# Optimization experiments

Measured on AMD Instinct MI355X. Metric: run time of the kernel, lower is better.

## Reference

```python
import jax, jax.numpy as jnp
import numpy as np

N0, N1, N2, N3 = 262144, 65536, 16384, 4096
EPS = 1e-5  # BatchNorm1d default eps


def setup_inputs() -> dict:
    key = jax.random.key(0)
    ks = jax.random.split(key, 10)
    f0 = jax.random.normal(ks[0], (N0, 64), dtype=jnp.float32)
    f1 = jax.random.normal(ks[1], (N1, 128), dtype=jnp.float32)
    f2 = jax.random.normal(ks[2], (N2, 256), dtype=jnp.float32)
    f3 = jax.random.normal(ks[3], (N3, 512), dtype=jnp.float32)
    # upsampling indices: finer level gathers from coarser level
    idx0 = jax.random.randint(ks[4], (N2,), 0, N3, dtype=jnp.int32)   # f3 -> level2
    idx1 = jax.random.randint(ks[5], (N1,), 0, N2, dtype=jnp.int32)   # f2 -> level1
    idx2 = jax.random.randint(ks[6], (N0,), 0, N1, dtype=jnp.int32)   # f1 -> level0
    # BN weight init'd to constant 0.25 in the module; bias defaults to 0
    bn_w2, bn_b2 = jnp.full((512,), 0.25, jnp.float32), jnp.zeros((512,), jnp.float32)
    bn_w1, bn_b1 = jnp.full((256,), 0.25, jnp.float32), jnp.zeros((256,), jnp.float32)
    bn_w0, bn_b0 = jnp.full((128,), 0.25, jnp.float32), jnp.zeros((128,), jnp.float32)
    # Linear(in, out, bias=False) weights, torch layout [out, in]
    W2 = jax.random.normal(ks[7], (256, 512), dtype=jnp.float32) * 0.02
    W1 = jax.random.normal(ks[8], (128, 256), dtype=jnp.float32) * 0.02
    W0 = jax.random.normal(ks[9], (64, 128), dtype=jnp.float32) * 0.02
    return dict(f0=f0, f1=f1, f2=f2, f3=f3,
                bn_w2=bn_w2, bn_b2=bn_b2, W2=W2,
                bn_w1=bn_w1, bn_b1=bn_b1, W1=W1,
                bn_w0=bn_w0, bn_b0=bn_b0, W0=W0,
                idx0=idx0, idx1=idx1, idx2=idx2)


def _decode(f, bn_w, bn_b, W):
    # BatchNorm1d (training-mode batch stats, biased variance) -> Linear (no bias)
    mean = jnp.mean(f, axis=0)
    var = jnp.var(f, axis=0)
    xn = (f - mean) * jax.lax.rsqrt(var + EPS)
    return (xn * bn_w + bn_b) @ W.T  # [N, out_ch]


def reference(f0, f1, f2, f3, bn_w2, bn_b2, W2, bn_w1, bn_b1, W1,
              bn_w0, bn_b0, W0, idx0, idx1, idx2):
    # gather (upsample) -> BN -> Linear -> residual add, coarse to fine
    f2 = f2 + _decode(f3[idx0], bn_w2, bn_b2, W2)   # [N2, 256]
    f1 = f1 + _decode(f2[idx1], bn_w1, bn_b1, W1)   # [N1, 128]
    f0 = f0 + _decode(f1[idx2], bn_w0, bn_b0, W0)   # [N0, 64]
    return f0
```

## Files before the change

### kernel.cpp

```cpp
#include <hip/hip_runtime.h>
#include <hip/hip_cooperative_groups.h>

namespace cg = cooperative_groups;

#define BN_EPS 1e-5f

constexpr int PN0 = 262144, PN1 = 65536, PN2 = 16384, PN3 = 4096;
constexpr int NBLK = 256, NTHR = 256;
constexpr size_t MB = 1u << 20;

typedef __attribute__((ext_vector_type(8))) short short8;
typedef __attribute__((ext_vector_type(4))) float f32x4;
typedef __attribute__((ext_vector_type(4))) unsigned int u32x4;

typedef const __attribute__((address_space(1))) unsigned int gu32;
typedef __attribute__((address_space(3))) unsigned int lu32;

__device__ __forceinline__ unsigned f2bf(float f) {
    unsigned u = __builtin_bit_cast(unsigned, f);
    u += 0x7fff + ((u >> 16) & 1);
    return u >> 16;
}
__device__ __forceinline__ float bf2f(unsigned h) {
    return __builtin_bit_cast(float, h << 16);
}
__device__ __forceinline__ f32x4 ntload4(const float* p) {
    return __builtin_nontemporal_load(reinterpret_cast<const f32x4*>(p));
}
__device__ __forceinline__ void ntstore4(float* p, f32x4 v) {
    __builtin_nontemporal_store(v, reinterpret_cast<f32x4*>(p));
}

struct MegaArgs {
    const float *f0, *f1, *f2, *f3;
    const float *bnw2, *bnb2, *W2;
    const float *bnw1, *bnb1, *W1;
    const float *bnw0, *bnb0, *W0;
    const int *idx0, *idx1, *idx2;
    unsigned short *f3bf, *dec2, *dec1, *dec0, *f2p, *f1p, *Wp2, *Wp1, *Wp0;
    int *cnt3, *cnt2, *cnt1;
    float *part2, *part1, *part0;
    float *d2, *d1, *d0;
    float *out;
};

template<int G, int NL>
__device__ __forceinline__ void red_write(float* aux, const float s[8], const float q[8],
                                          int tid, int lr, int cgi,
                                          float* part, int vb, int C) {
    #pragma unroll
    for (int j = 0; j < 8; ++j) aux[(lr * G + cgi) * 8 + j] = s[j];
    __syncthreads();
    if (tid < G) {
        float ss[8] = {};
        for (int l = 0; l < NL; ++l)
            #pragma unroll
            for (int j = 0; j < 8; ++j) ss[j] += aux[(l * G + tid) * 8 + j];
        #pragma unroll
        for (int j = 0; j < 8; ++j)
            part[((size_t)vb * C + tid * 8 + j) * 2] = ss[j];
    }
    __syncthreads();
    #pragma unroll
    for (int j = 0; j < 8; ++j) aux[(lr * G + cgi) * 8 + j] = q[j];
    __syncthreads();
    if (tid < G) {
        float qq[8] = {};
        for (int l = 0; l < NL; ++l)
            #pragma unroll
            for (int j = 0; j < 8; ++j) qq[j] += aux[(l * G + tid) * 8 + j];
        #pragma unroll
        for (int j = 0; j < 8; ++j)
            part[((size_t)vb * C + tid * 8 + j) * 2 + 1] = qq[j];
    }
    __syncthreads();
}

__device__ void phase_hist(const MegaArgs& a, int bid, int tid) {
    if (bid < 64) {
        atomicAdd(&a.cnt3[a.idx0[bid * NTHR + tid]], 1);
    } else {
        int t = (bid - 64) * NTHR + tid;
        atomicAdd(&a.cnt2[a.idx1[t]], 1);
        int t2 = t + 49152;
        if (t2 < PN1) atomicAdd(&a.cnt2[a.idx1[t2]], 1);
    }
}

__device__ void phase_stats(const MegaArgs& a, int bid, int tid, float* aux) {
    if (bid < 128) {
        const int cgi = tid & 63, lr = tid >> 6;
        const int r0 = bid * 32;
        float s[8] = {}, q[8] = {};
        #pragma unroll
        for (int i = 0; i < 8; ++i) {
            int r = r0 + lr + 4 * i;
            float w = (float)a.cnt3[r];
            const float* p = a.f3 + (size_t)r * 512 + cgi * 8;
            float4 x0 = *reinterpret_cast<const float4*>(p);
            float4 x1 = *reinterpret_cast<const float4*>(p + 4);
            float v[8] = {x0.x, x0.y, x0.z, x0.w, x1.x, x1.y, x1.z, x1.w};
            uint4 o;
            o.x = f2bf(v[0]) | (f2bf(v[1]) << 16);
            o.y = f2bf(v[2]) | (f2bf(v[3]) << 16);
            o.z = f2bf(v[4]) | (f2bf(v[5]) << 16);
            o.w = f2bf(v[6]) | (f2bf(v[7]) << 16);
            *reinterpret_cast<uint4*>(a.f3bf + (size_t)r * 512 + cgi * 8) = o;
            #pragma unroll
            for (int j = 0; j < 8; ++j) { s[j] += w * v[j]; q[j] += w * v[j] * v[j]; }
        }
        red_write<64, 4>(aux, s, q, tid, lr, cgi, a.part2, bid, 512);
    } else {
        int base = (bid - 128) * 2048;
        #pragma unroll
        for (int i = 0; i < 8; ++i)
            atomicAdd(&a.cnt1[a.idx2[base + i * NTHR + tid]], 1);
    }
}

template<int K, int NB>
__device__ void prep_phase(int bid, int tid, const float* part,
                           const float* bnw, const float* bnb, float invN,
                           const float* W, unsigned short* Wp, float* d,
                           float* aux) {
    float* sc = aux;
    float* sh = aux + K;
    for (int c = tid; c < K; c += NTHR) {
        float s = 0.f, q = 0.f;
        for (int b = 0; b < NB; ++b) {
            float2 p = *reinterpret_cast<const float2*>(part + ((size_t)b * K + c) * 2);
            s += p.x;
            q += p.y;
        }
        float mean = s * invN;
        float var = fmaxf(q * invN - mean * mean, 0.f);
        float scl = bnw[c] * rsqrtf(var + BN_EPS);
        sc[c] = scl;
        sh[c] = bnb[c] - mean * scl;
    }
    __syncthreads();
    const int nl = tid >> 4;
    const int kc = tid & 15;
    const int n = bid * 16 + nl;
    const int cb = n >> 6, n64 = n & 63;
    const float* wrow = W + (size_t)n * K;
    unsigned short* wp = Wp + (size_t)cb * 64 * K;
    float dp = 0.f;
    #pragma unroll
    for (int i = 0; i < K / 128; ++i) {
        int k = kc * 8 + i * 128;
        float4 w0 = *reinterpret_cast<const float4*>(wrow + k);
        float4 w1 = *reinterpret_cast<const float4*>(wrow + k + 4);
        float4 s0 = *reinterpret_cast<const float4*>(&sc[k]);
        float4 s1 = *reinterpret_cast<const float4*>(&sc[k + 4]);
        float4 h0 = *reinterpret_cast<const float4*>(&sh[k]);
        float4 h1 = *reinterpret_cast<const float4*>(&sh[k + 4]);
        dp += h0.x * w0.x + h0.y * w0.y + h0.z * w0.z + h0.w * w0.w
            + h1.x * w1.x + h1.y * w1.y + h1.z * w1.z + h1.w * w1.w;
        uint4 o;
        o.x = f2bf(w0.x * s0.x) | (f2bf(w0.y * s0.y) << 16);
        o.y = f2bf(w0.z * s0.z) | (f2bf(w0.w * s0.w) << 16);
        o.z = f2bf(w1.x * s1.x) | (f2bf(w1.y * s1.y) << 16);
        o.w = f2bf(w1.z * s1.z) | (f2bf(w1.w * s1.w) << 16);
        int si = (n64 * K + k) ^ ((n64 & 7) << 3);
        *reinterpret_cast<uint4*>(wp + si) = o;
    }
    dp += __shfl_xor(dp, 1); dp += __shfl_xor(dp, 2);
    dp += __shfl_xor(dp, 4); dp += __shfl_xor(dp, 8);
    if (kc == 0) d[n] = dp;
}

template<int K, int C>
__device__ void gemm_one(int chunk, int panel, int tid,
                         const unsigned short* src, const unsigned short* Wp,
                         const float* dvec, unsigned short* dec,
                         unsigned short* Wl) {
    constexpr int KK = K / 32;
    constexpr int CH = K / 8;
    const int lane = tid & 63;
    const int wv = tid >> 6;
    const int l15 = lane & 15, lg = lane >> 4;
    const int ncol0 = panel * 64;

    {
        const char* g = (const char*)(Wp + (size_t)panel * 64 * K);
        char* l = (char*)Wl;
        #pragma unroll
        for (int i = 0; i < CH / 4; ++i) {
            int ch = i * 4 + wv;
            __builtin_amdgcn_global_load_lds((gu32*)(g + ch * 1024 + lane * 16),
                                             (lu32*)(l + ch * 1024 + lane * 16), 16, 0, 0);
        }
    }

    const int row = chunk * 64 + wv * 16 + l15;
    const unsigned short* xp = src + (size_t)row * K + lg * 8;
    short8 xf[KK];
    #pragma unroll
    for (int kk = 0; kk < KK; ++kk)
        xf[kk] = *reinterpret_cast<const short8*>(xp + kk * 32);

    float4 dr[4];
    #pragma unroll
    for (int ni = 0; ni < 4; ++ni)
        dr[ni] = *reinterpret_cast<const float4*>(&dvec[ncol0 + ni * 16 + lg * 4]);

    __syncthreads();

    f32x4 acc[4];
    #pragma unroll
    for (int ni = 0; ni < 4; ++ni) acc[ni] = (f32x4){0.f, 0.f, 0.f, 0.f};
    #pragma unroll
    for (int kk = 0; kk < KK; ++kk) {
        #pragma unroll
        for (int ni = 0; ni < 4; ++ni) {
            const int si = ((ni * 16 + l15) * K + kk * 32 + lg * 8) ^ ((l15 & 7) << 3);
            short8 wf = *reinterpret_cast<const short8*>(&Wl[si]);
            acc[ni] = __builtin_amdgcn_mfma_f32_16x16x32_bf16(wf, xf[kk], acc[ni], 0, 0, 0);
        }
    }

    const size_t rowoff = (size_t)row * C + ncol0;
    #pragma unroll
    for (int ni = 0; ni < 4; ++ni) {
        size_t off = rowoff + ni * 16 + lg * 4;
        float v0 = dr[ni].x + acc[ni][0];
        float v1 = dr[ni].y + acc[ni][1];
        float v2 = dr[ni].z + acc[ni][2];
        float v3 = dr[ni].w + acc[ni][3];
        *reinterpret_cast<uint2*>(&dec[off]) =
            make_uint2(f2bf(v0) | (f2bf(v1) << 16), f2bf(v2) | (f2bf(v3) << 16));
    }
}

__device__ void phase_gemm1(const MegaArgs& a, int bid, int tid, unsigned short* Wl) {
    constexpr int K = 256;
    const int lane = tid & 63;
    const int wv = tid >> 6;
    const int l15 = lane & 15, lg = lane >> 4;

    {
        const char* g = (const char*)a.Wp1;
        char* l = (char*)Wl;
        #pragma unroll
        for (int i = 0; i < 16; ++i) {
            int ch = i * 4 + wv;
            __builtin_amdgcn_global_load_lds((gu32*)(g + ch * 1024 + lane * 16),
                                             (lu32*)(l + ch * 1024 + lane * 16), 16, 0, 0);
        }
    }

    const int row = bid * 64 + wv * 16 + l15;
    const unsigned short* xp = a.f2p + (size_t)row * K + lg * 8;
    short8 xf[8];
    #pragma unroll
    for (int kk = 0; kk < 8; ++kk)
        xf[kk] = *reinterpret_cast<const short8*>(xp + kk * 32);

    __syncthreads();

    #pragma unroll
    for (int p = 0; p < 2; ++p) {
        const unsigned short* wb = Wl + p * 64 * K;
        f32x4 acc[4];
        #pragma unroll
        for (int ni = 0; ni < 4; ++ni) acc[ni] = (f32x4){0.f, 0.f, 0.f, 0.f};
        #pragma unroll
        for (int kk = 0; kk < 8; ++kk) {
            #pragma unroll
            for (int ni = 0; ni < 4; ++ni) {
                const int si = ((ni * 16 + l15) * K + kk * 32 + lg * 8) ^ ((l15 & 7) << 3);
                short8 wf = *reinterpret_cast<const short8*>(&wb[si]);
                acc[ni] = __builtin_amdgcn_mfma_f32_16x16x32_bf16(wf, xf[kk], acc[ni], 0, 0, 0);
            }
        }
        const int ncol0 = p * 64;
        const size_t rowoff = (size_t)row * 128 + ncol0;
        #pragma unroll
        for (int ni = 0; ni < 4; ++ni) {
            float4 dr = *reinterpret_cast<const float4*>(&a.d1[ncol0 + ni * 16 + lg * 4]);
            size_t off = rowoff + ni * 16 + lg * 4;
            float v0 = dr.x + acc[ni][0];
            float v1 = dr.y + acc[ni][1];
            float v2 = dr.z + acc[ni][2];
            float v3 = dr.w + acc[ni][3];
            *reinterpret_cast<uint2*>(&a.dec1[off]) =
                make_uint2(f2bf(v0) | (f2bf(v1) << 16), f2bf(v2) | (f2bf(v3) << 16));
        }
    }
}

__device__ void phase_gemm0(const MegaArgs& a, int bid, int tid, unsigned short* Wl) {
    constexpr int K = 128;
    const int lane = tid & 63;
    const int wv = tid >> 6;
    const int l15 = lane & 15, lg = lane >> 4;

    {
        const char* g = (const char*)a.Wp0;
        char* l = (char*)Wl;
        #pragma unroll
        for (int i = 0; i < 4; ++i) {
            int ch = i * 4 + wv;
            __builtin_amdgcn_global_load_lds((gu32*)(g + ch * 1024 + lane * 16),
                                             (lu32*)(l + ch * 1024 + lane * 16), 16, 0, 0);
        }
    }
    float4 dr[4];
    #pragma unroll
    for (int ni = 0; ni < 4; ++ni)
        dr[ni] = *reinterpret_cast<const float4*>(&a.d0[ni * 16 + lg * 4]);
    __syncthreads();

    #pragma unroll
    for (int c = 0; c < 4; ++c) {
        const int row = (bid * 4 + c) * 64 + wv * 16 + l15;
        const unsigned short* xp = a.f1p + (size_t)row * K + lg * 8;
        short8 xf[4];
        #pragma unroll
        for (int kk = 0; kk < 4; ++kk)
            xf[kk] = *reinterpret_cast<const short8*>(xp + kk * 32);
        f32x4 acc[4];
        #pragma unroll
        for (int ni = 0; ni < 4; ++ni) acc[ni] = (f32x4){0.f, 0.f, 0.f, 0.f};
        #pragma unroll
        for (int kk = 0; kk < 4; ++kk) {
            #pragma unroll
            for (int ni = 0; ni < 4; ++ni) {
                const int si = ((ni * 16 + l15) * K + kk * 32 + lg * 8) ^ ((l15 & 7) << 3);
                short8 wf = *reinterpret_cast<const short8*>(&Wl[si]);
                acc[ni] = __builtin_amdgcn_mfma_f32_16x16x32_bf16(wf, xf[kk], acc[ni], 0, 0, 0);
            }
        }
        const size_t rowoff = (size_t)row * 64;
        #pragma unroll
        for (int ni = 0; ni < 4; ++ni) {
            size_t off = rowoff + ni * 16 + lg * 4;
            float v0 = dr[ni].x + acc[ni][0];
            float v1 = dr[ni].y + acc[ni][1];
            float v2 = dr[ni].z + acc[ni][2];
            float v3 = dr[ni].w + acc[ni][3];
            *reinterpret_cast<uint2*>(&a.dec0[off]) =
                make_uint2(f2bf(v0) | (f2bf(v1) << 16), f2bf(v2) | (f2bf(v3) << 16));
        }
    }
}

template<int C, int IT, bool STATS, bool OUT_F32>
__device__ void ga_phase(int vb, int tid, const float* base,
                         const unsigned short* dec, const int* idx,
                         const int* cnt_next, void* outv, float* part,
                         float* aux) {
    constexpr int G = C / 8;
    constexpr int NL = 256 / G;
    const int cgi = tid % G;
    const int lr = tid / G;
    const int r0 = vb * (NL * IT);

    int g[IT];
    #pragma unroll
    for (int i = 0; i < IT; ++i) g[i] = idx[r0 + lr + NL * i];

    float wreg[IT];
    if constexpr (STATS) {
        #pragma unroll
        for (int i = 0; i < IT; ++i) wreg[i] = (float)cnt_next[r0 + lr + NL * i];
    }

    u32x4 dv[IT];
    #pragma unroll
    for (int i = 0; i < IT; ++i)
        dv[i] = *reinterpret_cast<const u32x4*>(dec + (size_t)g[i] * C + cgi * 8);

    f32x4 b0[IT], b1[IT];
    #pragma unroll
    for (int i = 0; i < IT; ++i) {
        const float* bp = base + (size_t)(r0 + lr + NL * i) * C + cgi * 8;
        b0[i] = ntload4(bp);
        b1[i] = ntload4(bp + 4);
    }

    float s[8] = {}, q[8] = {};
    #pragma unroll
    for (int i = 0; i < IT; ++i) {
        const int r = r0 + lr + NL * i;
        float v[8];
        v[0] = b0[i][0] + bf2f(dv[i][0] & 0xffffu);
        v[1] = b0[i][1] + bf2f(dv[i][0] >> 16);
        v[2] = b0[i][2] + bf2f(dv[i][1] & 0xffffu);
        v[3] = b0[i][3] + bf2f(dv[i][1] >> 16);
        v[4] = b1[i][0] + bf2f(dv[i][2] & 0xffffu);
        v[5] = b1[i][1] + bf2f(dv[i][2] >> 16);
        v[6] = b1[i][2] + bf2f(dv[i][3] & 0xffffu);
        v[7] = b1[i][3] + bf2f(dv[i][3] >> 16);
        if constexpr (OUT_F32) {
            float* op = (float*)outv + (size_t)r * C + cgi * 8;
            ntstore4(op, (f32x4){v[0], v[1], v[2], v[3]});
            ntstore4(op + 4, (f32x4){v[4], v[5], v[6], v[7]});
        } else {
            unsigned h[8];
            #pragma unroll
            for (int j = 0; j < 8; ++j) h[j] = f2bf(v[j]);
            u32x4 o = {h[0] | (h[1] << 16), h[2] | (h[3] << 16),
                       h[4] | (h[5] << 16), h[6] | (h[7] << 16)};
            *reinterpret_cast<u32x4*>((unsigned short*)outv + (size_t)r * C + cgi * 8) = o;
            if constexpr (STATS) {
                #pragma unroll
                for (int j = 0; j < 8; ++j) {
                    float rv = bf2f(h[j]);
                    s[j] += wreg[i] * rv;
                    q[j] += wreg[i] * rv * rv;
                }
            }
        }
    }

    if constexpr (STATS)
        red_write<G, NL>(aux, s, q, tid, lr, cgi, part, vb, C);
}

__global__ __launch_bounds__(NTHR, 1) void mega(MegaArgs a) {
    __shared__ unsigned short Wl[64 * 512];
    __shared__ float aux[2048];
    cg::grid_group gg = cg::this_grid();
    const int bid = blockIdx.x;
    const int tid = threadIdx.x;

    phase_hist(a, bid, tid);
    __threadfence(); gg.sync(); __threadfence();

    phase_stats(a, bid, tid, aux);
    __threadfence(); gg.sync(); __threadfence();

    if (bid < 16)
        prep_phase<512, 128>(bid, tid, a.part2, a.bnw2, a.bnb2, 1.f / PN2, a.W2, a.Wp2, a.d2, aux);
    __threadfence(); gg.sync(); __threadfence();

    gemm_one<512, 256>(bid & 63, bid >> 6, tid, a.f3bf, a.Wp2, a.d2, a.dec2, Wl);
    __threadfence(); gg.sync(); __threadfence();

    ga_phase<256, 4, true, false>(bid * 2, tid, a.f2, a.dec2, a.idx0, a.cnt2, a.f2p, a.part1, aux);
    ga_phase<256, 4, true, false>(bid * 2 + 1, tid, a.f2, a.dec2, a.idx0, a.cnt2, a.f2p, a.part1, aux);
    __threadfence(); gg.sync(); __threadfence();

    if (bid < 8)
        prep_phase<256, 512>(bid, tid, a.part1, a.bnw1, a.bnb1, 1.f / PN1, a.W1, a.Wp1, a.d1, aux);
    __threadfence(); gg.sync(); __threadfence();

    phase_gemm1(a, bid, tid, Wl);
    __threadfence(); gg.sync(); __threadfence();

    ga_phase<128, 8, true, false>(bid * 2, tid, a.f1, a.dec1, a.idx1, a.cnt1, a.f1p, a.part0, aux);
    ga_phase<128, 8, true, false>(bid * 2 + 1, tid, a.f1, a.dec1, a.idx1, a.cnt1, a.f1p, a.part0, aux);
    __threadfence(); gg.sync(); __threadfence();

    if (bid < 4)
        prep_phase<128, 512>(bid, tid, a.part0, a.bnw0, a.bnb0, 1.f / PN0, a.W0, a.Wp0, a.d0, aux);
    __threadfence(); gg.sync(); __threadfence();

    phase_gemm0(a, bid, tid, Wl);
    __threadfence(); gg.sync(); __threadfence();

    #pragma unroll
    for (int c = 0; c < 4; ++c)
        ga_phase<64, 8, false, true>(bid * 4 + c, tid, a.f0, a.dec0, a.idx2, nullptr, a.out,
                                     nullptr, aux);
}

__global__ __launch_bounds__(NTHR) void k_hist(MegaArgs a) {
    phase_hist(a, blockIdx.x, threadIdx.x);
}
__global__ __launch_bounds__(NTHR) void k_stats(MegaArgs a) {
    __shared__ float aux[2048];
    phase_stats(a, blockIdx.x, threadIdx.x, aux);
}
template<int K, int NB>
__global__ __launch_bounds__(NTHR) void k_prep(const float* part, const float* bnw,
                                               const float* bnb, float invN, const float* W,
                                               unsigned short* Wp, float* d) {
    __shared__ float aux[2048];
    prep_phase<K, NB>(blockIdx.x, threadIdx.x, part, bnw, bnb, invN, W, Wp, d, aux);
}
__global__ __launch_bounds__(NTHR) void k_gemm2(MegaArgs a) {
    __shared__ unsigned short Wl[64 * 512];
    gemm_one<512, 256>(blockIdx.x & 63, blockIdx.x >> 6, threadIdx.x, a.f3bf, a.Wp2, a.d2,
                       a.dec2, Wl);
}
__global__ __launch_bounds__(NTHR) void k_gemm1(MegaArgs a) {
    __shared__ unsigned short Wl[64 * 512];
    phase_gemm1(a, blockIdx.x, threadIdx.x, Wl);
}
__global__ __launch_bounds__(NTHR) void k_gemm0(MegaArgs a) {
    __shared__ unsigned short Wl[64 * 128];
    phase_gemm0(a, blockIdx.x, threadIdx.x, Wl);
}
__global__ __launch_bounds__(NTHR) void k_ga2(MegaArgs a) {
    __shared__ float aux[2048];
    ga_phase<256, 4, true, false>(blockIdx.x * 2, threadIdx.x, a.f2, a.dec2, a.idx0, a.cnt2,
                                  a.f2p, a.part1, aux);
    ga_phase<256, 4, true, false>(blockIdx.x * 2 + 1, threadIdx.x, a.f2, a.dec2, a.idx0, a.cnt2,
                                  a.f2p, a.part1, aux);
}
__global__ __launch_bounds__(NTHR) void k_ga1(MegaArgs a) {
    __shared__ float aux[2048];
    ga_phase<128, 8, true, false>(blockIdx.x * 2, threadIdx.x, a.f1, a.dec1, a.idx1, a.cnt1,
                                  a.f1p, a.part0, aux);
    ga_phase<128, 8, true, false>(blockIdx.x * 2 + 1, threadIdx.x, a.f1, a.dec1, a.idx1, a.cnt1,
                                  a.f1p, a.part0, aux);
}
__global__ __launch_bounds__(NTHR) void k_ga0(MegaArgs a) {
    #pragma unroll
    for (int c = 0; c < 4; ++c)
        ga_phase<64, 8, false, true>(blockIdx.x * 4 + c, threadIdx.x, a.f0, a.dec0, a.idx2,
                                     nullptr, a.out, nullptr, nullptr);
}

extern "C" void kernel_launch(void* const* d_in, const int* in_sizes, int n_in,
                              void* d_out, int out_size, void* d_ws, size_t ws_size,
                              hipStream_t stream) {
    char* wsb = (char*)d_ws;
    unsigned short* f3bf = (unsigned short*)wsb;
    unsigned short* dec2 = (unsigned short*)(wsb + 4 * MB);
    unsigned short* dec1 = (unsigned short*)(wsb + 6 * MB);
    unsigned short* dec0 = (unsigned short*)(wsb + 10 * MB);
    unsigned short* f2p  = (unsigned short*)(wsb + 18 * MB);
    unsigned short* f1p  = (unsigned short*)(wsb + 26 * MB);
    unsigned short* Wp2  = (unsigned short*)(wsb + 42 * MB);
    unsigned short* Wp1  = Wp2 + 4 * 64 * 512;
    unsigned short* Wp0  = Wp1 + 2 * 64 * 256;
    int* cnt3 = (int*)(Wp0 + 64 * 128);
    int* cnt2 = cnt3 + PN3;
    int* cnt1 = cnt2 + PN2;
    float* part2 = (float*)(cnt1 + PN1);
    float* part1 = part2 + 256 * 512 * 2;
    float* part0 = part1 + 512 * 256 * 2;
    float* d2 = part0 + 1024 * 128 * 2;
    float* d1 = d2 + 256;
    float* d0 = d1 + 128;

    MegaArgs a;
    a.f0 = (const float*)d_in[0];
    a.f1 = (const float*)d_in[1];
    a.f2 = (const float*)d_in[2];
    a.f3 = (const float*)d_in[3];
    a.bnw2 = (const float*)d_in[4];
    a.bnb2 = (const float*)d_in[5];
    a.W2 = (const float*)d_in[6];
    a.bnw1 = (const float*)d_in[7];
    a.bnb1 = (const float*)d_in[8];
    a.W1 = (const float*)d_in[9];
    a.bnw0 = (const float*)d_in[10];
    a.bnb0 = (const float*)d_in[11];
    a.W0 = (const float*)d_in[12];
    a.idx0 = (const int*)d_in[13];
    a.idx1 = (const int*)d_in[14];
    a.idx2 = (const int*)d_in[15];
    a.f3bf = f3bf; a.dec2 = dec2; a.dec1 = dec1; a.dec0 = dec0;
    a.f2p = f2p; a.f1p = f1p; a.Wp2 = Wp2; a.Wp1 = Wp1; a.Wp0 = Wp0;
    a.cnt3 = cnt3; a.cnt2 = cnt2; a.cnt1 = cnt1;
    a.part2 = part2; a.part1 = part1; a.part0 = part0;
    a.d2 = d2; a.d1 = d1; a.d0 = d0;
    a.out = (float*)d_out;

    hipMemsetAsync(cnt3, 0, (size_t)(PN3 + PN2 + PN1) * sizeof(int), stream);

    int dev = 0;
    hipGetDevice(&dev);
    int coop = 0;
    hipDeviceGetAttribute(&coop, hipDeviceAttributeCooperativeLaunch, dev);
    int maxb = 0;
    hipOccupancyMaxActiveBlocksPerMultiprocessor(&maxb, mega, NTHR, 0);

    if (coop && maxb >= 1) {
        void* kargs[] = {&a};
        hipLaunchCooperativeKernel((void*)mega, dim3(NBLK), dim3(NTHR), kargs, 0, stream);
    } else {
        k_hist<<<256, NTHR, 0, stream>>>(a);
        k_stats<<<256, NTHR, 0, stream>>>(a);
        k_prep<512, 128><<<16, NTHR, 0, stream>>>(a.part2, a.bnw2, a.bnb2, 1.f / PN2, a.W2,
                                                  a.Wp2, a.d2);
        k_gemm2<<<256, NTHR, 0, stream>>>(a);
        k_ga2<<<256, NTHR, 0, stream>>>(a);
        k_prep<256, 512><<<8, NTHR, 0, stream>>>(a.part1, a.bnw1, a.bnb1, 1.f / PN1, a.W1,
                                                 a.Wp1, a.d1);
        k_gemm1<<<256, NTHR, 0, stream>>>(a);
        k_ga1<<<256, NTHR, 0, stream>>>(a);
        k_prep<128, 512><<<4, NTHR, 0, stream>>>(a.part0, a.bnw0, a.bnb0, 1.f / PN0, a.W0,
                                                 a.Wp0, a.d0);
        k_gemm0<<<256, NTHR, 0, stream>>>(a);
        k_ga0<<<256, NTHR, 0, stream>>>(a);
    }
}
```

Before: 168.0 us.

## Raise cooperative grid occupancy with grid-stride phases and smaller LDS footprint

```diff
diff --git a/kernel.cpp b/kernel.cpp
--- a/kernel.cpp
+++ b/kernel.cpp
@@ -6,7 +6,7 @@
 #define BN_EPS 1e-5f
 
 constexpr int PN0 = 262144, PN1 = 65536, PN2 = 16384, PN3 = 4096;
-constexpr int NBLK = 256, NTHR = 256;
+constexpr int NTHR = 256;
 constexpr size_t MB = 1u << 20;
 
 typedef __attribute__((ext_vector_type(8))) short short8;
@@ -38,7 +38,7 @@
     const float *bnw0, *bnb0, *W0;
     const int *idx0, *idx1, *idx2;
     unsigned short *f3bf, *dec2, *dec1, *dec0, *f2p, *f1p, *Wp2, *Wp1, *Wp0;
-    int *cnt3, *cnt2, *cnt1;
+    int *cnt2, *cnt1;
     float *part2, *part1, *part0;
     float *d2, *d1, *d0;
     float *out;
@@ -76,45 +76,58 @@
     __syncthreads();
 }
 
-__device__ void phase_hist(const MegaArgs& a, int bid, int tid) {
-    if (bid < 64) {
-        atomicAdd(&a.cnt3[a.idx0[bid * NTHR + tid]], 1);
-    } else {
-        int t = (bid - 64) * NTHR + tid;
-        atomicAdd(&a.cnt2[a.idx1[t]], 1);
-        int t2 = t + 49152;
-        if (t2 < PN1) atomicAdd(&a.cnt2[a.idx1[t2]], 1);
-    }
-}
-
-__device__ void phase_stats(const MegaArgs& a, int bid, int tid, float* aux) {
-    if (bid < 128) {
-        const int cgi = tid & 63, lr = tid >> 6;
-        const int r0 = bid * 32;
-        float s[8] = {}, q[8] = {};
-        #pragma unroll
-        for (int i = 0; i < 8; ++i) {
-            int r = r0 + lr + 4 * i;
-            float w = (float)a.cnt3[r];
-            const float* p = a.f3 + (size_t)r * 512 + cgi * 8;
-            float4 x0 = *reinterpret_cast<const float4*>(p);
-            float4 x1 = *reinterpret_cast<const float4*>(p + 4);
-            float v[8] = {x0.x, x0.y, x0.z, x0.w, x1.x, x1.y, x1.z, x1.w};
-            uint4 o;
-            o.x = f2bf(v[0]) | (f2bf(v[1]) << 16);
-            o.y = f2bf(v[2]) | (f2bf(v[3]) << 16);
-            o.z = f2bf(v[4]) | (f2bf(v[5]) << 16);
-            o.w = f2bf(v[6]) | (f2bf(v[7]) << 16);
-            *reinterpret_cast<uint4*>(a.f3bf + (size_t)r * 512 + cgi * 8) = o;
+__device__ void stats_gathered(const MegaArgs& a, int vb, int tid, float* aux) {
+    const int cgi = tid & 63, lr = tid >> 6;
+    const int r0 = vb * 128;
+    float s[8] = {}, q[8] = {};
+    for (int i = 0; i < 32; ++i) {
+        int r = r0 + lr + 4 * i;
+        int gi = a.idx0[r];
+        const float* p = a.f3 + (size_t)gi * 512 + cgi * 8;
+        float4 x0 = *reinterpret_cast<const float4*>(p);
+        float4 x1 = *reinterpret_cast<const float4*>(p + 4);
+        float v[8] = {x0.x, x0.y, x0.z, x0.w, x1.x, x1.y, x1.z, x1.w};
+        #pragma unroll
+        for (int j = 0; j < 8; ++j) { s[j] += v[j]; q[j] += v[j] * v[j]; }
+    }
+    red_write<64, 4>(aux, s, q, tid, lr, cgi, a.part2, vb, 512);
+}
+
+__device__ void cvt_f3(const MegaArgs& a, int vb, int tid) {
+    const int cgi = tid & 63, lr = tid >> 6;
+    const int r0 = vb * 32;
+    #pragma unroll
+    for (int i = 0; i < 8; ++i) {
+        int r = r0 + lr + 4 * i;
+        const float* p = a.f3 + (size_t)r * 512 + cgi * 8;
+        float4 x0 = *reinterpret_cast<const float4*>(p);
+        float4 x1 = *reinterpret_cast<const float4*>(p + 4);
+        uint4 o;
+        o.x = f2bf(x0.x) | (f2bf(x0.y) << 16);
+        o.y = f2bf(x0.z) | (f2bf(x0.w) << 16);
+        o.z = f2bf(x1.x) | (f2bf(x1.y) << 16);
+        o.w = f2bf(x1.z) | (f2bf(x1.w) << 16);
+        *reinterpret_cast<uint4*>(a.f3bf + (size_t)r * 512 + cgi * 8) = o;
+    }
+}
+
+__device__ void phase1(const MegaArgs& a, int nb, int bid, int tid, float* aux) {
+    for (int vb = bid; vb < 416; vb += nb) {
+        if (vb < 128) {
+            stats_gathered(a, vb, tid, aux);
+        } else if (vb < 256) {
+            cvt_f3(a, vb - 128, tid);
+        } else if (vb < 288) {
+            int b = vb - 256;
             #pragma unroll
-            for (int j = 0; j < 8; ++j) { s[j] += w * v[j]; q[j] += w * v[j] * v[j]; }
-        }
-        red_write<64, 4>(aux, s, q, tid, lr, cgi, a.part2, bid, 512);
-    } else {
-        int base = (bid - 128) * 2048;
-        #pragma unroll
-        for (int i = 0; i < 8; ++i)
-            atomicAdd(&a.cnt1[a.idx2[base + i * NTHR + tid]], 1);
+            for (int i = 0; i < 8; ++i)
+                atomicAdd(&a.cnt2[a.idx1[b * 2048 + i * NTHR + tid]], 1);
+        } else {
+            int b = vb - 288;
+            #pragma unroll
+            for (int i = 0; i < 8; ++i)
+                atomicAdd(&a.cnt1[a.idx2[b * 2048 + i * NTHR + tid]], 1);
+        }
     }
 }
 
@@ -168,6 +181,86 @@
     dp += __shfl_xor(dp, 1); dp += __shfl_xor(dp, 2);
     dp += __shfl_xor(dp, 4); dp += __shfl_xor(dp, 8);
     if (kc == 0) d[n] = dp;
+    __syncthreads();
+}
+
+__device__ void gemm2_one(int chunk, int panel, int tid,
+                          const unsigned short* src, const unsigned short* Wp,
+                          const float* dvec, unsigned short* dec,
+                          unsigned short* Wl) {
+    constexpr int K = 512;
+    const int lane = tid & 63;
+    const int wv = tid >> 6;
+    const int l15 = lane & 15, lg = lane >> 4;
+    const char* gbase = (const char*)(Wp + (size_t)panel * 64 * K);
+    char* lbase = (char*)Wl;
+
+    #pragma unroll
+    for (int i = 0; i < 8; ++i) {
+        int ch = i * 4 + wv;
+        __builtin_amdgcn_global_load_lds((gu32*)(gbase + ch * 1024 + lane * 16),
+                                         (lu32*)(lbase + ch * 1024 + lane * 16), 16, 0, 0);
+    }
+
+    const int row = chunk * 64 + wv * 16 + l15;
+    const unsigned short* xp = src + (size_t)row * K + lg * 8;
+    short8 xf[16];
+    #pragma unroll
+    for (int kk = 0; kk < 16; ++kk)
+        xf[kk] = *reinterpret_cast<const short8*>(xp + kk * 32);
+
+    float4 dr[4];
+    #pragma unroll
+    for (int ni = 0; ni < 4; ++ni)
+        dr[ni] = *reinterpret_cast<const float4*>(&dvec[panel * 64 + ni * 16 + lg * 4]);
+
+    __syncthreads();
+
+    f32x4 acc[4];
+    #pragma unroll
+    for (int ni = 0; ni < 4; ++ni) acc[ni] = (f32x4){0.f, 0.f, 0.f, 0.f};
+
+    #pragma unroll
+    for (int kk = 0; kk < 16; ++kk) {
+        #pragma unroll
+        for (int ni = 0; ni < 2; ++ni) {
+            const int si = ((ni * 16 + l15) * K + kk * 32 + lg * 8) ^ ((l15 & 7) << 3);
+            short8 wf = *reinterpret_cast<const short8*>(&Wl[si]);
+            acc[ni] = __builtin_amdgcn_mfma_f32_16x16x32_bf16(wf, xf[kk], acc[ni], 0, 0, 0);
+        }
+    }
+    __syncthreads();
+
+    #pragma unroll
+    for (int i = 0; i < 8; ++i) {
+        int ch = i * 4 + wv;
+        __builtin_amdgcn_global_load_lds((gu32*)(gbase + 32768 + ch * 1024 + lane * 16),
+                                         (lu32*)(lbase + ch * 1024 + lane * 16), 16, 0, 0);
+    }
+    __syncthreads();
+
+    #pragma unroll
+    for (int kk = 0; kk < 16; ++kk) {
+        #pragma unroll
+        for (int ni = 0; ni < 2; ++ni) {
+            const int si = ((ni * 16 + l15) * K + kk * 32 + lg * 8) ^ ((l15 & 7) << 3);
+            short8 wf = *reinterpret_cast<const short8*>(&Wl[si]);
+            acc[2 + ni] = __builtin_amdgcn_mfma_f32_16x16x32_bf16(wf, xf[kk], acc[2 + ni], 0, 0, 0);
+        }
+    }
+
+    const size_t rowoff = (size_t)row * 256 + panel * 64;
+    #pragma unroll
+    for (int ni = 0; ni < 4; ++ni) {
+        size_t off = rowoff + ni * 16 + lg * 4;
+        float v0 = dr[ni].x + acc[ni][0];
+        float v1 = dr[ni].y + acc[ni][1];
+        float v2 = dr[ni].z + acc[ni][2];
+        float v3 = dr[ni].w + acc[ni][3];
+        *reinterpret_cast<uint2*>(&dec[off]) =
+            make_uint2(f2bf(v0) | (f2bf(v1) << 16), f2bf(v2) | (f2bf(v3) << 16));
+    }
+    __syncthreads();
 }
 
 template<int K, int C>
@@ -231,66 +324,10 @@
         *reinterpret_cast<uint2*>(&dec[off]) =
             make_uint2(f2bf(v0) | (f2bf(v1) << 16), f2bf(v2) | (f2bf(v3) << 16));
     }
-}
-
-__device__ void phase_gemm1(const MegaArgs& a, int bid, int tid, unsigned short* Wl) {
-    constexpr int K = 256;
-    const int lane = tid & 63;
-    const int wv = tid >> 6;
-    const int l15 = lane & 15, lg = lane >> 4;
-
-    {
-        const char* g = (const char*)a.Wp1;
-        char* l = (char*)Wl;
-        #pragma unroll
-        for (int i = 0; i < 16; ++i) {
-            int ch = i * 4 + wv;
-            __builtin_amdgcn_global_load_lds((gu32*)(g + ch * 1024 + lane * 16),
-                                             (lu32*)(l + ch * 1024 + lane * 16), 16, 0, 0);
-        }
-    }
-
-    const int row = bid * 64 + wv * 16 + l15;
-    const unsigned short* xp = a.f2p + (size_t)row * K + lg * 8;
-    short8 xf[8];
-    #pragma unroll
-    for (int kk = 0; kk < 8; ++kk)
-        xf[kk] = *reinterpret_cast<const short8*>(xp + kk * 32);
-
-    __syncthreads();
-
-    #pragma unroll
-    for (int p = 0; p < 2; ++p) {
-        const unsigned short* wb = Wl + p * 64 * K;
-        f32x4 acc[4];
-        #pragma unroll
-        for (int ni = 0; ni < 4; ++ni) acc[ni] = (f32x4){0.f, 0.f, 0.f, 0.f};
-        #pragma unroll
-        for (int kk = 0; kk < 8; ++kk) {
-            #pragma unroll
-            for (int ni = 0; ni < 4; ++ni) {
-                const int si = ((ni * 16 + l15) * K + kk * 32 + lg * 8) ^ ((l15 & 7) << 3);
-                short8 wf = *reinterpret_cast<const short8*>(&wb[si]);
-                acc[ni] = __builtin_amdgcn_mfma_f32_16x16x32_bf16(wf, xf[kk], acc[ni], 0, 0, 0);
-            }
-        }
-        const int ncol0 = p * 64;
-        const size_t rowoff = (size_t)row * 128 + ncol0;
-        #pragma unroll
-        for (int ni = 0; ni < 4; ++ni) {
-            float4 dr = *reinterpret_cast<const float4*>(&a.d1[ncol0 + ni * 16 + lg * 4]);
-            size_t off = rowoff + ni * 16 + lg * 4;
-            float v0 = dr.x + acc[ni][0];
-            float v1 = dr.y + acc[ni][1];
-            float v2 = dr.z + acc[ni][2];
-            float v3 = dr.w + acc[ni][3];
-            *reinterpret_cast<uint2*>(&a.dec1[off]) =
-                make_uint2(f2bf(v0) | (f2bf(v1) << 16), f2bf(v2) | (f2bf(v3) << 16));
-        }
-    }
-}
-
-__device__ void phase_gemm0(const MegaArgs& a, int bid, int tid, unsigned short* Wl) {
+    __syncthreads();
+}
+
+__device__ void phase_gemm0(const MegaArgs& a, int nb, int bid, int tid, unsigned short* Wl) {
     constexpr int K = 128;
     const int lane = tid & 63;
     const int wv = tid >> 6;
@@ -312,9 +349,8 @@
         dr[ni] = *reinterpret_cast<const float4*>(&a.d0[ni * 16 + lg * 4]);
     __syncthreads();
 
-    #pragma unroll
-    for (int c = 0; c < 4; ++c) {
-        const int row = (bid * 4 + c) * 64 + wv * 16 + l15;
+    for (int vb = bid; vb < 1024; vb += nb) {
+        const int row = vb * 64 + wv * 16 + l15;
         const unsigned short* xp = a.f1p + (size_t)row * K + lg * 8;
         short8 xf[4];
         #pragma unroll
@@ -419,60 +455,57 @@
         red_write<G, NL>(aux, s, q, tid, lr, cgi, part, vb, C);
 }
 
-__global__ __launch_bounds__(NTHR, 1) void mega(MegaArgs a) {
-    __shared__ unsigned short Wl[64 * 512];
+#define FENCE_SYNC { __threadfence(); gg.sync(); __threadfence(); }
+
+__global__ __launch_bounds__(NTHR, 3) void mega(MegaArgs a) {
+    __shared__ unsigned short Wl[64 * 256];
     __shared__ float aux[2048];
     cg::grid_group gg = cg::this_grid();
+    const int nb = gridDim.x;
     const int bid = blockIdx.x;
     const int tid = threadIdx.x;
 
-    phase_hist(a, bid, tid);
-    __threadfence(); gg.sync(); __threadfence();
-
-    phase_stats(a, bid, tid, aux);
-    __threadfence(); gg.sync(); __threadfence();
-
-    if (bid < 16)
-        prep_phase<512, 128>(bid, tid, a.part2, a.bnw2, a.bnb2, 1.f / PN2, a.W2, a.Wp2, a.d2, aux);
-    __threadfence(); gg.sync(); __threadfence();
-
-    gemm_one<512, 256>(bid & 63, bid >> 6, tid, a.f3bf, a.Wp2, a.d2, a.dec2, Wl);
-    __threadfence(); gg.sync(); __threadfence();
-
-    ga_phase<256, 4, true, false>(bid * 2, tid, a.f2, a.dec2, a.idx0, a.cnt2, a.f2p, a.part1, aux);
-    ga_phase<256, 4, true, false>(bid * 2 + 1, tid, a.f2, a.dec2, a.idx0, a.cnt2, a.f2p, a.part1, aux);
-    __threadfence(); gg.sync(); __threadfence();
-
-    if (bid < 8)
-        prep_phase<256, 512>(bid, tid, a.part1, a.bnw1, a.bnb1, 1.f / PN1, a.W1, a.Wp1, a.d1, aux);
-    __threadfence(); gg.sync(); __threadfence();
-
-    phase_gemm1(a, bid, tid, Wl);
-    __threadfence(); gg.sync(); __threadfence();
-
-    ga_phase<128, 8, true, false>(bid * 2, tid, a.f1, a.dec1, a.idx1, a.cnt1, a.f1p, a.part0, aux);
-    ga_phase<128, 8, true, false>(bid * 2 + 1, tid, a.f1, a.dec1, a.idx1, a.cnt1, a.f1p, a.part0, aux);
-    __threadfence(); gg.sync(); __threadfence();
-
-    if (bid < 4)
-        prep_phase<128, 512>(bid, tid, a.part0, a.bnw0, a.bnb0, 1.f / PN0, a.W0, a.Wp0, a.d0, aux);
-    __threadfence(); gg.sync(); __threadfence();
-
-    phase_gemm0(a, bid, tid, Wl);
-    __threadfence(); gg.sync(); __threadfence();
-
-    #pragma unroll
-    for (int c = 0; c < 4; ++c)
-        ga_phase<64, 8, false, true>(bid * 4 + c, tid, a.f0, a.dec0, a.idx2, nullptr, a.out,
-                                     nullptr, aux);
-}
-
-__global__ __launch_bounds__(NTHR) void k_hist(MegaArgs a) {
-    phase_hist(a, blockIdx.x, threadIdx.x);
-}
-__global__ __launch_bounds__(NTHR) void k_stats(MegaArgs a) {
+    phase1(a, nb, bid, tid, aux);
+    FENCE_SYNC;
+
+    for (int vb = bid; vb < 16; vb += nb)
+        prep_phase<512, 128>(vb, tid, a.part2, a.bnw2, a.bnb2, 1.f / PN2, a.W2, a.Wp2, a.d2, aux);
+    FENCE_SYNC;
+
+    for (int vb = bid; vb < 256; vb += nb)
+        gemm2_one(vb & 63, vb >> 6, tid, a.f3bf, a.Wp2, a.d2, a.dec2, Wl);
+    FENCE_SYNC;
+
+    for (int vb = bid; vb < 512; vb += nb)
+        ga_phase<256, 4, true, false>(vb, tid, a.f2, a.dec2, a.idx0, a.cnt2, a.f2p, a.part1, aux);
+    FENCE_SYNC;
+
+    for (int vb = bid; vb < 8; vb += nb)
+        prep_phase<256, 512>(vb, tid, a.part1, a.bnw1, a.bnb1, 1.f / PN1, a.W1, a.Wp1, a.d1, aux);
+    FENCE_SYNC;
+
+    for (int vb = bid; vb < 512; vb += nb)
+        gemm_one<256, 128>(vb >> 1, vb & 1, tid, a.f2p, a.Wp1, a.d1, a.dec1, Wl);
+    FENCE_SYNC;
+
+    for (int vb = bid; vb < 512; vb += nb)
+        ga_phase<128, 8, true, false>(vb, tid, a.f1, a.dec1, a.idx1, a.cnt1, a.f1p, a.part0, aux);
+    FENCE_SYNC;
+
+    for (int vb = bid; vb < 4; vb += nb)
+        prep_phase<128, 512>(vb, tid, a.part0, a.bnw0, a.bnb0, 1.f / PN0, a.W0, a.Wp0, a.d0, aux);
+    FENCE_SYNC;
+
+    phase_gemm0(a, nb, bid, tid, Wl);
+    FENCE_SYNC;
+
+    for (int vb = bid; vb < 1024; vb += nb)
+        ga_phase<64, 8, false, true>(vb, tid, a.f0, a.dec0, a.idx2, nullptr, a.out, nullptr, aux);
+}
+
+__global__ __launch_bounds__(NTHR) void k_p1(MegaArgs a) {
     __shared__ float aux[2048];
-    phase_stats(a, blockIdx.x, threadIdx.x, aux);
+    phase1(a, gridDim.x, blockIdx.x, threadIdx.x, aux);
 }
 template<int K, int NB>
 __global__ __launch_bounds__(NTHR) void k_prep(const float* part, const float* bnw,
@@ -482,37 +515,35 @@
     prep_phase<K, NB>(blockIdx.x, threadIdx.x, part, bnw, bnb, invN, W, Wp, d, aux);
 }
 __global__ __launch_bounds__(NTHR) void k_gemm2(MegaArgs a) {
-    __shared__ unsigned short Wl[64 * 512];
-    gemm_one<512, 256>(blockIdx.x & 63, blockIdx.x >> 6, threadIdx.x, a.f3bf, a.Wp2, a.d2,
-                       a.dec2, Wl);
+    __shared__ unsigned short Wl[64 * 256];
+    for (int vb = blockIdx.x; vb < 256; vb += gridDim.x)
+        gemm2_one(vb & 63, vb >> 6, threadIdx.x, a.f3bf, a.Wp2, a.d2, a.dec2, Wl);
 }
 __global__ __launch_bounds__(NTHR) void k_gemm1(MegaArgs a) {
-    __shared__ unsigned short Wl[64 * 512];
-    phase_gemm1(a, blockIdx.x, threadIdx.x, Wl);
+    __shared__ unsigned short Wl[64 * 256];
+    for (int vb = blockIdx.x; vb < 512; vb += gridDim.x)
+        gemm_one<256, 128>(vb >> 1, vb & 1, threadIdx.x, a.f2p, a.Wp1, a.d1, a.dec1, Wl);
 }
 __global__ __launch_bounds__(NTHR) void k_gemm0(MegaArgs a) {
     __shared__ unsigned short Wl[64 * 128];
-    phase_gemm0(a, blockIdx.x, threadIdx.x, Wl);
+    phase_gemm0(a, gridDim.x, blockIdx.x, threadIdx.x, Wl);
 }
 __global__ __launch_bounds__(NTHR) void k_ga2(MegaArgs a) {
     __shared__ float aux[2048];
-    ga_phase<256, 4, true, false>(blockIdx.x * 2, threadIdx.x, a.f2, a.dec2, a.idx0, a.cnt2,
-                                  a.f2p, a.part1, aux);
-    ga_phase<256, 4, true, false>(blockIdx.x * 2 + 1, threadIdx.x, a.f2, a.dec2, a.idx0, a.cnt2,
-                                  a.f2p, a.part1, aux);
+    for (int vb = blockIdx.x; vb < 512; vb += gridDim.x)
+        ga_phase<256, 4, true, false>(vb, threadIdx.x, a.f2, a.dec2, a.idx0, a.cnt2,
+                                      a.f2p, a.part1, aux);
 }
 __global__ __launch_bounds__(NTHR) void k_ga1(MegaArgs a) {
     __shared__ float aux[2048];
-    ga_phase<128, 8, true, false>(blockIdx.x * 2, threadIdx.x, a.f1, a.dec1, a.idx1, a.cnt1,
-                                  a.f1p, a.part0, aux);
-    ga_phase<128, 8, true, false>(blockIdx.x * 2 + 1, threadIdx.x, a.f1, a.dec1, a.idx1, a.cnt1,
-                                  a.f1p, a.part0, aux);
+    for (int vb = blockIdx.x; vb < 512; vb += gridDim.x)
+        ga_phase<128, 8, true, false>(vb, threadIdx.x, a.f1, a.dec1, a.idx1, a.cnt1,
+                                      a.f1p, a.part0, aux);
 }
 __global__ __launch_bounds__(NTHR) void k_ga0(MegaArgs a) {
-    #pragma unroll
-    for (int c = 0; c < 4; ++c)
-        ga_phase<64, 8, false, true>(blockIdx.x * 4 + c, threadIdx.x, a.f0, a.dec0, a.idx2,
-                                     nullptr, a.out, nullptr, nullptr);
+    for (int vb = blockIdx.x; vb < 1024; vb += gridDim.x)
+        ga_phase<64, 8, false, true>(vb, threadIdx.x, a.f0, a.dec0, a.idx2, nullptr,
+                                     a.out, nullptr, nullptr);
 }
 
 extern "C" void kernel_launch(void* const* d_in, const int* in_sizes, int n_in,
@@ -528,13 +559,12 @@
     unsigned short* Wp2  = (unsigned short*)(wsb + 42 * MB);
     unsigned short* Wp1  = Wp2 + 4 * 64 * 512;
     unsigned short* Wp0  = Wp1 + 2 * 64 * 256;
-    int* cnt3 = (int*)(Wp0 + 64 * 128);
-    int* cnt2 = cnt3 + PN3;
+    int* cnt2 = (int*)(Wp0 + 64 * 128);
     int* cnt1 = cnt2 + PN2;
     float* part2 = (float*)(cnt1 + PN1);
-    float* part1 = part2 + 256 * 512 * 2;
+    float* part1 = part2 + 128 * 512 * 2;
     float* part0 = part1 + 512 * 256 * 2;
-    float* d2 = part0 + 1024 * 128 * 2;
+    float* d2 = part0 + 512 * 128 * 2;
     float* d1 = d2 + 256;
     float* d0 = d1 + 128;
 
@@ -557,12 +587,12 @@
     a.idx2 = (const int*)d_in[15];
     a.f3bf = f3bf; a.dec2 = dec2; a.dec1 = dec1; a.dec0 = dec0;
     a.f2p = f2p; a.f1p = f1p; a.Wp2 = Wp2; a.Wp1 = Wp1; a.Wp0 = Wp0;
-    a.cnt3 = cnt3; a.cnt2 = cnt2; a.cnt1 = cnt1;
+    a.cnt2 = cnt2; a.cnt1 = cnt1;
     a.part2 = part2; a.part1 = part1; a.part0 = part0;
     a.d2 = d2; a.d1 = d1; a.d0 = d0;
     a.out = (float*)d_out;
 
-    hipMemsetAsync(cnt3, 0, (size_t)(PN3 + PN2 + PN1) * sizeof(int), stream);
+    hipMemsetAsync(cnt2, 0, (size_t)(PN2 + PN1) * sizeof(int), stream);
 
     int dev = 0;
     hipGetDevice(&dev);
@@ -572,22 +602,23 @@
     hipOccupancyMaxActiveBlocksPerMultiprocessor(&maxb, mega, NTHR, 0);
 
     if (coop && maxb >= 1) {
+        int nblk = maxb * 256;
+        if (nblk > 1024) nblk = 1024;
         void* kargs[] = {&a};
-        hipLaunchCooperativeKernel((void*)mega, dim3(NBLK), dim3(NTHR), kargs, 0, stream);
+        hipLaunchCooperativeKernel((void*)mega, dim3(nblk), dim3(NTHR), kargs, 0, stream);
     } else {
-        k_hist<<<256, NTHR, 0, stream>>>(a);
-        k_stats<<<256, NTHR, 0, stream>>>(a);
+        k_p1<<<416, NTHR, 0, stream>>>(a);
         k_prep<512, 128><<<16, NTHR, 0, stream>>>(a.part2, a.bnw2, a.bnb2, 1.f / PN2, a.W2,
                                                   a.Wp2, a.d2);
         k_gemm2<<<256, NTHR, 0, stream>>>(a);
-        k_ga2<<<256, NTHR, 0, stream>>>(a);
+        k_ga2<<<512, NTHR, 0, stream>>>(a);
         k_prep<256, 512><<<8, NTHR, 0, stream>>>(a.part1, a.bnw1, a.bnb1, 1.f / PN1, a.W1,
                                                  a.Wp1, a.d1);
-        k_gemm1<<<256, NTHR, 0, stream>>>(a);
-        k_ga1<<<256, NTHR, 0, stream>>>(a);
+        k_gemm1<<<512, NTHR, 0, stream>>>(a);
+        k_ga1<<<512, NTHR, 0, stream>>>(a);
         k_prep<128, 512><<<4, NTHR, 0, stream>>>(a.part0, a.bnw0, a.bnb0, 1.f / PN0, a.W0,
                                                  a.Wp0, a.d0);
-        k_gemm0<<<256, NTHR, 0, stream>>>(a);
-        k_ga0<<<256, NTHR, 0, stream>>>(a);
-    }
-}
+        k_gemm0<<<768, NTHR, 0, stream>>>(a);
+        k_ga0<<<1024, NTHR, 0, stream>>>(a);
+    }
+}
```

Result: no change. 168.2 us (+0.1%).
